# Optimization experiments

Measured on AMD Instinct MI355X. Metric: run time of the kernel, lower is better.

## Reference

```python
import jax, jax.numpy as jnp
import numpy as np

# Model dims: H features, N half-state-size, R low-rank, CH output channels, KL kernel length
H, N, R, CH, KL = 512, 64, 1, 1, 4096


def setup_inputs() -> dict:
    key = jax.random.key(0)
    ks = jax.random.split(key, 8)
    log_dt = jax.random.uniform(ks[0], (H,), minval=float(np.log(1e-3)), maxval=float(np.log(1e-1)), dtype=jnp.float32)
    # Hurwitz-like poles: negative real part, HiPPO-like imaginary ladder
    w_re = -0.5 - jax.random.uniform(ks[1], (H, N), dtype=jnp.float32)
    w_im = jnp.broadcast_to(np.float32(np.pi) * jnp.arange(N, dtype=jnp.float32), (H, N))
    B_re = jax.random.normal(ks[2], (1, H, N), dtype=jnp.float32)
    B_im = jax.random.normal(ks[3], (1, H, N), dtype=jnp.float32)
    # small low-rank correction keeps the Woodbury denominator away from zero
    P_re = 0.1 * jax.random.normal(ks[4], (R, H, N), dtype=jnp.float32)
    P_im = 0.1 * jax.random.normal(ks[5], (R, H, N), dtype=jnp.float32)
    C_re = jax.random.normal(ks[6], (CH, H, N), dtype=jnp.float32)
    C_im = jax.random.normal(ks[7], (CH, H, N), dtype=jnp.float32)
    return dict(log_dt=log_dt, w_re=w_re, w_im=w_im, B_re=B_re, B_im=B_im,
                P_re=P_re, P_im=P_im, C_re=C_re, C_im=C_im, L=KL)


def _kernel(log_dt, w_re, w_im, B_re, B_im, P_re, P_im, C_re, C_im, L):
    dt = jnp.exp(log_dt)                                   # (H,)
    w = (w_re + 1j * w_im) * dt[:, None]                   # (H,N) discretized poles w*dt
    B = B_re + 1j * B_im                                   # (1,H,N)
    P = P_re + 1j * P_im                                   # (R,H,N)
    Q = jnp.conj(P)                                        # hurwitz=False path: Q = conj(P)
    C = C_re + 1j * C_im                                   # (CH,H,N)

    Lf = L // 2 + 1
    kk = jnp.arange(Lf)
    omega = jnp.exp((-2j * np.pi) * kk / L)                # FFT roots of unity (complex64)
    den = 1.0 + omega
    # Nyquist node (omega = -1) handled analytically below; guard the division
    safe_den = jnp.where(jnp.abs(den) < 1e-6, jnp.ones_like(den), den)
    z = 2.0 * (1.0 - omega) / safe_den                     # bilinear-transform nodes

    Bc = jnp.concatenate([B, P], axis=0)                   # (1+R,H,N)
    Cc = jnp.concatenate([C, Q], axis=0)                   # (CH+R,H,N)
    v = Bc[:, None] * Cc[None]                             # (1+R,CH+R,H,N)

    # Cauchy kernel: r[a,b,h,l] = sum_n v[a,b,h,n] / (z[l] - w[h,n])
    recip = 1.0 / (z[None, None, :] - w[:, :, None])       # (H,N,Lf)
    r = jnp.einsum('abhn,hnl->abhl', v, recip)             # (1+R,CH+R,H,Lf)
    r = r * dt[None, None, :, None]

    # rank-1 Woodbury correction
    k_f = r[:-1, :-1] - r[:-1, -1:] * r[-1:, :-1] / (1.0 + r[-1:, -1:])
    k_f = k_f * 2.0 / safe_den

    if L % 2 == 0:
        # analytic z -> inf limit at the Nyquist node: dt/2 * sum_n v00
        nyq = 0.5 * dt[None, None, :] * jnp.sum(v[:-1, :-1], axis=-1)  # (1,CH,H)
        k_f = k_f.at[..., -1].set(nyq)

    k = jnp.fft.irfft(k_f, n=L, axis=-1)[..., :L]          # (1,CH,H,L) real
    return k[-1]                                           # (CH,H,L)


def reference(log_dt, w_re, w_im, B_re, B_im, P_re, P_im, C_re, C_im, L):
    return _kernel(log_dt, w_re, w_im, B_re, B_im, P_re, P_im, C_re, C_im, L)
```

## Files before the change

### kernel.cpp

```cpp
#include <hip/hip_runtime.h>
#include <hip/hip_bf16.h>
#include <math.h>


#define HH   512
#define NN   64
#define LLEN 4096
#define MM   2048
#define NTHREADS 1024
#define ZPAD(i) ((i) + ((i) >> 4))

typedef float v2f __attribute__((ext_vector_type(2)));

__global__ __launch_bounds__(NTHREADS, 8) void ssknplr_kernel(
    const float* __restrict__ log_dt,
    const float* __restrict__ w_re, const float* __restrict__ w_im,
    const float* __restrict__ B_re, const float* __restrict__ B_im,
    const float* __restrict__ P_re, const float* __restrict__ P_im,
    const float* __restrict__ C_re, const float* __restrict__ C_im,
    float* __restrict__ out)
{
    __shared__ v2f    s_pp[NN][10];
    __shared__ float2 s_Z[ZPAD(MM) + 1];

    const int h   = blockIdx.x;
    const int tid = threadIdx.x;

    if (tid < NN) {
        const int n   = tid;
        const int idx = h * NN + n;
        const float dt = expf(log_dt[h]);
        const float wr = w_re[idx] * dt;
        const float wi = w_im[idx] * dt;
        const float Br = B_re[idx], Bi = B_im[idx];
        const float Pr = P_re[idx], Pi = P_im[idx];
        const float Cr = C_re[idx], Ci = C_im[idx];
        const float vals[10] = {
            -wi, -wr, wr * wr,
            dt * (Br * Cr - Bi * Ci),
            dt * (Br * Ci + Bi * Cr),
            dt * (Br * Pr + Bi * Pi),
            dt * (Bi * Pr - Br * Pi),
            dt * (Pr * Cr - Pi * Ci),
            dt * (Pr * Ci + Pi * Cr),
            dt * (Pr * Pr + Pi * Pi)
        };
        #pragma unroll
        for (int j = 0; j < 10; ++j) s_pp[n][j] = (v2f){vals[j], vals[j]};
    }
    __syncthreads();

    v2f tv;
    {
        const float rx = (float)tid * (1.0f / 8192.0f);
        const float ry = (float)(tid + 1024) * (1.0f / 8192.0f);
        tv.x = __builtin_amdgcn_sinf(rx) * __builtin_amdgcn_rcpf(__builtin_amdgcn_cosf(rx));
        tv.y = __builtin_amdgcn_sinf(ry) * __builtin_amdgcn_rcpf(__builtin_amdgcn_cosf(ry));
    }
    const v2f t2v = tv + tv;

    v2f a00r = 0.f, a00i = 0.f, a01r = 0.f, a01i = 0.f;
    v2f a10r = 0.f, a10i = 0.f, a11r = 0.f, a11i = 0.f;

    for (int n = 0; n < NN; ++n) {
        const v2f mwi  = s_pp[n][0];
        const v2f nr   = s_pp[n][1];
        const v2f wr2  = s_pp[n][2];
        const v2f dim = t2v + mwi;
        const v2f den = __builtin_elementwise_fma(dim, dim, wr2);
        const float ip = __builtin_amdgcn_rcpf(den.x * den.y);
        const v2f dsw = __builtin_shufflevector(den, den, 1, 0);
        const v2f inv = dsw * (v2f){ip, ip};
        const v2f ur = nr * inv;
        const v2f ui = -(dim * inv);
        const v2f v00r = s_pp[n][3], v00i = s_pp[n][4];
        const v2f v01r = s_pp[n][5], v01i = s_pp[n][6];
        const v2f v10r = s_pp[n][7], v10i = s_pp[n][8];
        const v2f v11  = s_pp[n][9];
        a00r = __builtin_elementwise_fma( v00r, ur, a00r);
        a00r = __builtin_elementwise_fma(-v00i, ui, a00r);
        a00i = __builtin_elementwise_fma( v00r, ui, a00i);
        a00i = __builtin_elementwise_fma( v00i, ur, a00i);
        a01r = __builtin_elementwise_fma( v01r, ur, a01r);
        a01r = __builtin_elementwise_fma(-v01i, ui, a01r);
        a01i = __builtin_elementwise_fma( v01r, ui, a01i);
        a01i = __builtin_elementwise_fma( v01i, ur, a01i);
        a10r = __builtin_elementwise_fma( v10r, ur, a10r);
        a10r = __builtin_elementwise_fma(-v10i, ui, a10r);
        a10i = __builtin_elementwise_fma( v10r, ui, a10i);
        a10i = __builtin_elementwise_fma( v10i, ur, a10i);
        a11r = __builtin_elementwise_fma( v11,  ur, a11r);
        a11i = __builtin_elementwise_fma( v11,  ui, a11i);
    }

    {
        const v2f dr = a11r + 1.0f;
        const v2f di = a11i;
        const v2f dd = __builtin_elementwise_fma(dr, dr, di * di);
        v2f dinv;
        dinv.x = __builtin_amdgcn_rcpf(dd.x);
        dinv.y = __builtin_amdgcn_rcpf(dd.y);
        const v2f numr = a01r * a10r - a01i * a10i;
        const v2f numi = a01r * a10i + a01i * a10r;
        const v2f cr = (numr * dr + numi * di) * dinv;
        const v2f ci = (numi * dr - numr * di) * dinv;
        const v2f Wr = a00r - cr;
        const v2f Wi = a00i - ci;
        const v2f Kr = __builtin_elementwise_fma(-tv, Wi, Wr);
        const v2f Ki = __builtin_elementwise_fma( tv, Wr, Wi);
        s_Z[ZPAD(tid)] = make_float2(Kr.x, (tid == 0) ? 0.0f : Ki.x);
        s_Z[ZPAD(tid + 1024)] = make_float2(Kr.y, Ki.y);
    }
    if (tid == 0) {
        float sr = 0.f;
        for (int n = 0; n < NN; ++n) sr += s_pp[n][3].x;
        s_Z[ZPAD(MM)] = make_float2(0.5f * sr, 0.0f);
    }
    __syncthreads();

    {
        const int k = tid;
        if (k == 0) {
            const float a = s_Z[ZPAD(0)].x;
            const float b = s_Z[ZPAD(MM)].x;
            s_Z[ZPAD(0)] = make_float2(0.5f * (a + b), 0.5f * (a - b));
            const float2 km = s_Z[ZPAD(MM / 2)];
            s_Z[ZPAD(MM / 2)] = make_float2(km.x, -km.y);
        } else {
            const float2 Ka = s_Z[ZPAD(k)];
            const float2 Kb = s_Z[ZPAD(MM - k)];
            const float rk = (float)k * (1.0f / 4096.0f);
            const float sk = __builtin_amdgcn_sinf(rk);
            const float ck = __builtin_amdgcn_cosf(rk);
            const float Pr = 0.5f * (Ka.x + Kb.x), Pi = 0.5f * (Ka.y - Kb.y);
            const float Dr = 0.5f * (Ka.x - Kb.x), Di = 0.5f * (Ka.y + Kb.y);
            const float al = sk * Dr + ck * Di;
            const float be = ck * Dr - sk * Di;
            s_Z[ZPAD(k)]      = make_float2(Pr - al, Pi + be);
            s_Z[ZPAD(MM - k)] = make_float2(Pr + al, be - Pi);
        }
    }
    __syncthreads();

    for (int s = 10; s >= 1; s -= 2) {
        const int H = 1 << s;
        const int Q = H >> 1;
        const float scale = __builtin_amdgcn_rcpf((float)(2 * H));
        if (tid < 512) {
            const int b    = tid;
            const int j    = b & (Q - 1);
            const int base = ((b >> (s - 1)) << (s + 1)) + j;
            const int i0 = base, i1 = base + Q, i2 = base + H, i3 = base + H + Q;
            const float rev = (float)j * scale;
            const float c  = __builtin_amdgcn_cosf(rev);
            const float sn = __builtin_amdgcn_sinf(rev);
            const float wbr = c * c - sn * sn;
            const float wbi = 2.0f * c * sn;
            const float2 u0 = s_Z[ZPAD(i0)];
            const float2 u1 = s_Z[ZPAD(i1)];
            const float2 u2 = s_Z[ZPAD(i2)];
            const float2 u3 = s_Z[ZPAD(i3)];
            const float a0r = u0.x + u2.x, a0i = u0.y + u2.y;
            const float d0r = u0.x - u2.x, d0i = u0.y - u2.y;
            const float a1r = u1.x + u3.x, a1i = u1.y + u3.y;
            const float d1r = u1.x - u3.x, d1i = u1.y - u3.y;
            const float e0r = d0r * c  - d0i * sn, e0i = d0r * sn + d0i * c;
            const float e1r = -(d1r * sn) - d1i * c, e1i = d1r * c - d1i * sn;
            s_Z[ZPAD(i0)] = make_float2(a0r + a1r, a0i + a1i);
            const float t0r = a0r - a1r, t0i = a0i - a1i;
            s_Z[ZPAD(i1)] = make_float2(t0r * wbr - t0i * wbi, t0r * wbi + t0i * wbr);
            s_Z[ZPAD(i2)] = make_float2(e0r + e1r, e0i + e1i);
            const float t1r = e0r - e1r, t1i = e0i - e1i;
            s_Z[ZPAD(i3)] = make_float2(t1r * wbr - t1i * wbi, t1r * wbi + t1i * wbr);
        }
        __syncthreads();
    }
    {
        const int i0 = tid << 1, i1 = i0 | 1;
        const float2 u = s_Z[ZPAD(i0)];
        const float2 v = s_Z[ZPAD(i1)];
        s_Z[ZPAD(i0)] = make_float2(u.x + v.x, u.y + v.y);
        s_Z[ZPAD(i1)] = make_float2(u.x - v.x, u.y - v.y);
    }
    __syncthreads();

    const float scale = 1.0f / (float)MM;
    float2* o2 = (float2*)out + (size_t)h * MM;
    #pragma unroll
    for (int q = 0; q < 2; ++q) {
        const int m = tid + q * NTHREADS;
        const int r = (int)(__brev((unsigned)m) >> 21);
        const float2 z = s_Z[ZPAD(r)];
        o2[m] = make_float2(z.x * scale, z.y * scale);
    }
}

extern "C" void kernel_launch(void* const* d_in, const int* in_sizes, int n_in,
                              void* d_out, int out_size, void* d_ws, size_t ws_size,
                              hipStream_t stream) {
    const float* log_dt = (const float*)d_in[0];
    const float* w_re   = (const float*)d_in[1];
    const float* w_im   = (const float*)d_in[2];
    const float* B_re   = (const float*)d_in[3];
    const float* B_im   = (const float*)d_in[4];
    const float* P_re   = (const float*)d_in[5];
    const float* P_im   = (const float*)d_in[6];
    const float* C_re   = (const float*)d_in[7];
    const float* C_im   = (const float*)d_in[8];
    float* out = (float*)d_out;

    ssknplr_kernel<<<dim3(HH), dim3(NTHREADS), 0, stream>>>(
        log_dt, w_re, w_im, B_re, B_im, P_re, P_im, C_re, C_im, out);
}
```

Measured before the change: 38.09 us.

## Split into Cauchy kernel and radix-8 register iFFT kernel via workspace

Splits the fused per-head kernel into two launches. A Cauchy kernel uses 1024 blocks of 256 threads, each thread computing four frequency nodes with two independent accumulator sets for more ILP, and writes the spectrum to workspace. A separate inverse-FFT kernel runs radix-8 stages in registers with fewer barriers. This adds a global round trip and a second launch in exchange for smaller blocks and better occupancy, and keeps the fused kernel as a fallback when the workspace is too small.

Result: slower. 42.01 us (+10.3%).

```diff
diff --git a/kernel.cpp b/kernel.cpp
--- a/kernel.cpp
+++ b/kernel.cpp
@@ -7,12 +7,308 @@
 #define NN   64
 #define LLEN 4096
 #define MM   2048
-#define NTHREADS 1024
+#define WS_STRIDE 2056
+#define ZP(i) ((i) + ((i) >> 4) + ((i) >> 8))
 #define ZPAD(i) ((i) + ((i) >> 4))
 
 typedef float v2f __attribute__((ext_vector_type(2)));
 
-__global__ __launch_bounds__(NTHREADS, 8) void ssknplr_kernel(
+__device__ __forceinline__ float sinr(float r) { return __builtin_amdgcn_sinf(r); }
+__device__ __forceinline__ float cosr(float r) { return __builtin_amdgcn_cosf(r); }
+__device__ __forceinline__ float rcpf(float x) { return __builtin_amdgcn_rcpf(x); }
+
+
+__device__ __forceinline__ void cauchy_step(
+    const v2f tv, const v2f mwi, const v2f nr, const v2f wr2,
+    const v2f v00r, const v2f v00i, const v2f v01r, const v2f v01i,
+    const v2f v10r, const v2f v10i, const v2f v11,
+    v2f& a00r, v2f& a00i, v2f& a01r, v2f& a01i,
+    v2f& a10r, v2f& a10i, v2f& a11r, v2f& a11i)
+{
+    const v2f dim = __builtin_elementwise_fma(tv, (v2f){2.0f, 2.0f}, mwi);
+    const v2f den = __builtin_elementwise_fma(dim, dim, wr2);
+    const float ip = rcpf(den.x * den.y);
+    v2f inv; inv.x = den.y * ip; inv.y = den.x * ip;
+    const v2f ur = nr * inv;
+    const v2f ui = -(dim * inv);
+    a00r = __builtin_elementwise_fma( v00r, ur, a00r);
+    a00r = __builtin_elementwise_fma(-v00i, ui, a00r);
+    a00i = __builtin_elementwise_fma( v00r, ui, a00i);
+    a00i = __builtin_elementwise_fma( v00i, ur, a00i);
+    a01r = __builtin_elementwise_fma( v01r, ur, a01r);
+    a01r = __builtin_elementwise_fma(-v01i, ui, a01r);
+    a01i = __builtin_elementwise_fma( v01r, ui, a01i);
+    a01i = __builtin_elementwise_fma( v01i, ur, a01i);
+    a10r = __builtin_elementwise_fma( v10r, ur, a10r);
+    a10r = __builtin_elementwise_fma(-v10i, ui, a10r);
+    a10i = __builtin_elementwise_fma( v10r, ui, a10i);
+    a10i = __builtin_elementwise_fma( v10i, ur, a10i);
+    a11r = __builtin_elementwise_fma( v11,  ur, a11r);
+    a11i = __builtin_elementwise_fma( v11,  ui, a11i);
+}
+
+__device__ __forceinline__ void woodbury_K(
+    const v2f tv,
+    const v2f a00r, const v2f a00i, const v2f a01r, const v2f a01i,
+    const v2f a10r, const v2f a10i, const v2f a11r, const v2f a11i,
+    v2f& Kr, v2f& Ki)
+{
+    const v2f dr = a11r + 1.0f;
+    const v2f di = a11i;
+    const v2f dd = __builtin_elementwise_fma(dr, dr, di * di);
+    v2f dinv; dinv.x = rcpf(dd.x); dinv.y = rcpf(dd.y);
+    const v2f numr = a01r * a10r - a01i * a10i;
+    const v2f numi = a01r * a10i + a01i * a10r;
+    const v2f cr = (numr * dr + numi * di) * dinv;
+    const v2f ci = (numi * dr - numr * di) * dinv;
+    const v2f Wr = a00r - cr;
+    const v2f Wi = a00i - ci;
+    Kr = __builtin_elementwise_fma(-tv, Wi, Wr);
+    Ki = __builtin_elementwise_fma( tv, Wr, Wi);
+}
+
+__global__ __launch_bounds__(256, 6) void cauchy_kernel(
+    const float* __restrict__ log_dt,
+    const float* __restrict__ w_re, const float* __restrict__ w_im,
+    const float* __restrict__ B_re, const float* __restrict__ B_im,
+    const float* __restrict__ P_re, const float* __restrict__ P_im,
+    const float* __restrict__ C_re, const float* __restrict__ C_im,
+    float2* __restrict__ Kout)
+{
+    __shared__ float4 s_p4[NN][5];
+
+    const int blk   = blockIdx.x;
+    const int h     = blk >> 1;
+    const int chunk = blk & 1;
+    const int tid   = threadIdx.x;
+
+    if (tid < NN) {
+        const int n   = tid;
+        const int idx = h * NN + n;
+        const float dt = expf(log_dt[h]);
+        const float wr = w_re[idx] * dt;
+        const float wi = w_im[idx] * dt;
+        const float Br = B_re[idx], Bi = B_im[idx];
+        const float Pr = P_re[idx], Pi = P_im[idx];
+        const float Cr = C_re[idx], Ci = C_im[idx];
+        const float v00r = dt * (Br * Cr - Bi * Ci);
+        const float v00i = dt * (Br * Ci + Bi * Cr);
+        const float v01r = dt * (Br * Pr + Bi * Pi);
+        const float v01i = dt * (Bi * Pr - Br * Pi);
+        const float v10r = dt * (Pr * Cr - Pi * Ci);
+        const float v10i = dt * (Pr * Ci + Pi * Cr);
+        const float v11  = dt * (Pr * Pr + Pi * Pi);
+        s_p4[n][0] = make_float4(-wi, -wi, -wr, -wr);
+        s_p4[n][1] = make_float4(wr * wr, wr * wr, v00r, v00r);
+        s_p4[n][2] = make_float4(v00i, v00i, v01r, v01r);
+        s_p4[n][3] = make_float4(v01i, v01i, v10r, v10r);
+        s_p4[n][4] = make_float4(v10i, v10i, v11, v11);
+    }
+    __syncthreads();
+
+    const int l0 = chunk * 256 + tid;
+    v2f tvA, tvB;
+    {
+        const float rA0 = (float)l0            * (1.0f / 8192.0f);
+        const float rA1 = (float)(l0 + 1024)   * (1.0f / 8192.0f);
+        const float rB0 = (float)(l0 + 512)    * (1.0f / 8192.0f);
+        const float rB1 = (float)(l0 + 1536)   * (1.0f / 8192.0f);
+        tvA.x = sinr(rA0) * rcpf(cosr(rA0));
+        tvA.y = sinr(rA1) * rcpf(cosr(rA1));
+        tvB.x = sinr(rB0) * rcpf(cosr(rB0));
+        tvB.y = sinr(rB1) * rcpf(cosr(rB1));
+    }
+
+    v2f A00r = 0.f, A00i = 0.f, A01r = 0.f, A01i = 0.f;
+    v2f A10r = 0.f, A10i = 0.f, A11r = 0.f, A11i = 0.f;
+    v2f B00r = 0.f, B00i = 0.f, B01r = 0.f, B01i = 0.f;
+    v2f B10r = 0.f, B10i = 0.f, B11r = 0.f, B11i = 0.f;
+
+    for (int n = 0; n < NN; ++n) {
+        const float4 f0 = s_p4[n][0];
+        const float4 f1 = s_p4[n][1];
+        const float4 f2 = s_p4[n][2];
+        const float4 f3 = s_p4[n][3];
+        const float4 f4 = s_p4[n][4];
+        const v2f mwi  = {f0.x, f0.y}, nr   = {f0.z, f0.w};
+        const v2f wr2  = {f1.x, f1.y}, v00r = {f1.z, f1.w};
+        const v2f v00i = {f2.x, f2.y}, v01r = {f2.z, f2.w};
+        const v2f v01i = {f3.x, f3.y}, v10r = {f3.z, f3.w};
+        const v2f v10i = {f4.x, f4.y}, v11  = {f4.z, f4.w};
+        cauchy_step(tvA, mwi, nr, wr2, v00r, v00i, v01r, v01i, v10r, v10i, v11,
+                    A00r, A00i, A01r, A01i, A10r, A10i, A11r, A11i);
+        cauchy_step(tvB, mwi, nr, wr2, v00r, v00i, v01r, v01i, v10r, v10i, v11,
+                    B00r, B00i, B01r, B01i, B10r, B10i, B11r, B11i);
+    }
+
+    float2* __restrict__ Kh = Kout + (size_t)h * WS_STRIDE;
+    {
+        v2f Kr, Ki;
+        woodbury_K(tvA, A00r, A00i, A01r, A01i, A10r, A10i, A11r, A11i, Kr, Ki);
+        Kh[l0]        = make_float2(Kr.x, (l0 == 0) ? 0.0f : Ki.x);
+        Kh[l0 + 1024] = make_float2(Kr.y, Ki.y);
+    }
+    {
+        v2f Kr, Ki;
+        woodbury_K(tvB, B00r, B00i, B01r, B01i, B10r, B10i, B11r, B11i, Kr, Ki);
+        Kh[l0 + 512]  = make_float2(Kr.x, Ki.x);
+        Kh[l0 + 1536] = make_float2(Kr.y, Ki.y);
+    }
+    if (chunk == 0 && tid == 0) {
+        float sr = 0.f;
+        for (int n = 0; n < NN; ++n) sr += s_p4[n][1].z;
+        Kh[MM] = make_float2(0.5f * sr, 0.0f);
+    }
+}
+
+
+__device__ __forceinline__ void radix8(float xr[8], float xi[8], const float rev)
+{
+    const float c   = cosr(rev), s = sinr(rev);
+    const float w2r = c * c - s * s, w2i = 2.0f * c * s;
+    const float w4r = w2r * w2r - w2i * w2i;
+    const float w4i = 2.0f * w2r * w2i;
+    const float RH  = 0.70710678118654752440f;
+    const float cms = RH * (c - s), cps = RH * (c + s);
+
+    const float Ar0 = xr[0] + xr[4], Ai0 = xi[0] + xi[4];
+    const float Ar1 = xr[1] + xr[5], Ai1 = xi[1] + xi[5];
+    const float Ar2 = xr[2] + xr[6], Ai2 = xi[2] + xi[6];
+    const float Ar3 = xr[3] + xr[7], Ai3 = xi[3] + xi[7];
+    float dr, di;
+    dr = xr[0] - xr[4]; di = xi[0] - xi[4];
+    const float Br0 = dr * c - di * s,      Bi0 = dr * s + di * c;
+    dr = xr[1] - xr[5]; di = xi[1] - xi[5];
+    const float Br1 = dr * cms - di * cps,  Bi1 = dr * cps + di * cms;
+    dr = xr[2] - xr[6]; di = xi[2] - xi[6];
+    const float Br2 = -dr * s - di * c,     Bi2 = dr * c - di * s;
+    dr = xr[3] - xr[7]; di = xi[3] - xi[7];
+    const float Br3 = -dr * cps - di * cms, Bi3 = dr * cms - di * cps;
+
+    const float Cr0 = Ar0 + Ar2, Ci0 = Ai0 + Ai2;
+    const float Cr1 = Ar1 + Ar3, Ci1 = Ai1 + Ai3;
+    dr = Ar0 - Ar2; di = Ai0 - Ai2;
+    const float Dr0 = dr * w2r - di * w2i,  Di0 = dr * w2i + di * w2r;
+    dr = Ar1 - Ar3; di = Ai1 - Ai3;
+    const float Dr1 = -dr * w2i - di * w2r, Di1 = dr * w2r - di * w2i;
+    const float Er0 = Br0 + Br2, Ei0 = Bi0 + Bi2;
+    const float Er1 = Br1 + Br3, Ei1 = Bi1 + Bi3;
+    dr = Br0 - Br2; di = Bi0 - Bi2;
+    const float Fr0 = dr * w2r - di * w2i,  Fi0 = dr * w2i + di * w2r;
+    dr = Br1 - Br3; di = Bi1 - Bi3;
+    const float Fr1 = -dr * w2i - di * w2r, Fi1 = dr * w2r - di * w2i;
+
+    xr[0] = Cr0 + Cr1; xi[0] = Ci0 + Ci1;
+    dr = Cr0 - Cr1; di = Ci0 - Ci1;
+    xr[1] = dr * w4r - di * w4i; xi[1] = dr * w4i + di * w4r;
+    xr[2] = Dr0 + Dr1; xi[2] = Di0 + Di1;
+    dr = Dr0 - Dr1; di = Di0 - Di1;
+    xr[3] = dr * w4r - di * w4i; xi[3] = dr * w4i + di * w4r;
+    xr[4] = Er0 + Er1; xi[4] = Ei0 + Ei1;
+    dr = Er0 - Er1; di = Ei0 - Ei1;
+    xr[5] = dr * w4r - di * w4i; xi[5] = dr * w4i + di * w4r;
+    xr[6] = Fr0 + Fr1; xi[6] = Fi0 + Fi1;
+    dr = Fr0 - Fr1; di = Fi0 - Fi1;
+    xr[7] = dr * w4r - di * w4i; xi[7] = dr * w4i + di * w4r;
+}
+
+__global__ __launch_bounds__(256, 2) void ifft_kernel(
+    const float2* __restrict__ Kg, float* __restrict__ out)
+{
+    __shared__ float2 s_Z[ZP(MM - 1) + 1];
+
+    const int h = blockIdx.x;
+    const int t = threadIdx.x;
+    const float2* __restrict__ Kh = Kg + (size_t)h * WS_STRIDE;
+
+    float xr[8], xi[8];
+
+    #pragma unroll
+    for (int q = 0; q < 8; ++q) {
+        const int m = t + (q << 8);
+        const float2 Ka = Kh[m];
+        const float2 Kb = Kh[MM - m];
+        const float rev = (float)m * (1.0f / 4096.0f);
+        const float sk = sinr(rev), ck = cosr(rev);
+        const float Pr = 0.5f * (Ka.x + Kb.x), Pi = 0.5f * (Ka.y - Kb.y);
+        const float Dr = 0.5f * (Ka.x - Kb.x), Di = 0.5f * (Ka.y + Kb.y);
+        xr[q] = Pr - (sk * Dr + ck * Di);
+        xi[q] = Pi + (ck * Dr - sk * Di);
+    }
+    radix8(xr, xi, (float)t * (1.0f / 2048.0f));
+    #pragma unroll
+    for (int q = 0; q < 8; ++q) {
+        const int i = t + (q << 8);
+        s_Z[ZP(i)] = make_float2(xr[q], xi[q]);
+    }
+    __syncthreads();
+
+    {
+        const int base = ((t >> 5) << 8) + (t & 31);
+        #pragma unroll
+        for (int q = 0; q < 8; ++q) {
+            const float2 z = s_Z[ZP(base + (q << 5))];
+            xr[q] = z.x; xi[q] = z.y;
+        }
+        radix8(xr, xi, (float)(t & 31) * (1.0f / 256.0f));
+        #pragma unroll
+        for (int q = 0; q < 8; ++q)
+            s_Z[ZP(base + (q << 5))] = make_float2(xr[q], xi[q]);
+    }
+    __syncthreads();
+
+    {
+        const int base = ((t >> 2) << 5) + (t & 3);
+        #pragma unroll
+        for (int q = 0; q < 8; ++q) {
+            const float2 z = s_Z[ZP(base + (q << 2))];
+            xr[q] = z.x; xi[q] = z.y;
+        }
+        radix8(xr, xi, (float)(t & 3) * (1.0f / 32.0f));
+        #pragma unroll
+        for (int q = 0; q < 8; ++q)
+            s_Z[ZP(base + (q << 2))] = make_float2(xr[q], xi[q]);
+    }
+    __syncthreads();
+
+    {
+        const int i0 = t << 3;
+        #pragma unroll
+        for (int q = 0; q < 8; ++q) {
+            const float2 z = s_Z[ZP(i0 + q)];
+            xr[q] = z.x; xi[q] = z.y;
+        }
+        #pragma unroll
+        for (int g = 0; g < 2; ++g) {
+            const int o = g * 4;
+            const float A0r = xr[o] + xr[o+2], A0i = xi[o] + xi[o+2];
+            const float A1r = xr[o+1] + xr[o+3], A1i = xi[o+1] + xi[o+3];
+            const float B0r = xr[o] - xr[o+2], B0i = xi[o] - xi[o+2];
+            const float B1r = -(xi[o+1] - xi[o+3]);
+            const float B1i =  (xr[o+1] - xr[o+3]);
+            xr[o]   = A0r + A1r; xi[o]   = A0i + A1i;
+            xr[o+1] = A0r - A1r; xi[o+1] = A0i - A1i;
+            xr[o+2] = B0r + B1r; xi[o+2] = B0i + B1i;
+            xr[o+3] = B0r - B1r; xi[o+3] = B0i - B1i;
+        }
+        #pragma unroll
+        for (int q = 0; q < 8; ++q)
+            s_Z[ZP(i0 + q)] = make_float2(xr[q], xi[q]);
+    }
+    __syncthreads();
+
+    const float scale = 1.0f / (float)MM;
+    float2* o2 = (float2*)out + (size_t)h * MM;
+    #pragma unroll
+    for (int q = 0; q < 8; ++q) {
+        const int m = t + (q << 8);
+        const int r = (int)(__brev((unsigned)m) >> 21);
+        const float2 z = s_Z[ZP(r)];
+        o2[m] = make_float2(z.x * scale, z.y * scale);
+    }
+}
+
+__global__ __launch_bounds__(1024, 8) void ssknplr_fused(
     const float* __restrict__ log_dt,
     const float* __restrict__ w_re, const float* __restrict__ w_im,
     const float* __restrict__ B_re, const float* __restrict__ B_im,
@@ -37,12 +333,9 @@
         const float Cr = C_re[idx], Ci = C_im[idx];
         const float vals[10] = {
             -wi, -wr, wr * wr,
-            dt * (Br * Cr - Bi * Ci),
-            dt * (Br * Ci + Bi * Cr),
-            dt * (Br * Pr + Bi * Pi),
-            dt * (Bi * Pr - Br * Pi),
-            dt * (Pr * Cr - Pi * Ci),
-            dt * (Pr * Ci + Pi * Cr),
+            dt * (Br * Cr - Bi * Ci), dt * (Br * Ci + Bi * Cr),
+            dt * (Br * Pr + Bi * Pi), dt * (Bi * Pr - Br * Pi),
+            dt * (Pr * Cr - Pi * Ci), dt * (Pr * Ci + Pi * Cr),
             dt * (Pr * Pr + Pi * Pi)
         };
         #pragma unroll
@@ -54,60 +347,19 @@
     {
         const float rx = (float)tid * (1.0f / 8192.0f);
         const float ry = (float)(tid + 1024) * (1.0f / 8192.0f);
-        tv.x = __builtin_amdgcn_sinf(rx) * __builtin_amdgcn_rcpf(__builtin_amdgcn_cosf(rx));
-        tv.y = __builtin_amdgcn_sinf(ry) * __builtin_amdgcn_rcpf(__builtin_amdgcn_cosf(ry));
-    }
-    const v2f t2v = tv + tv;
-
+        tv.x = sinr(rx) * rcpf(cosr(rx));
+        tv.y = sinr(ry) * rcpf(cosr(ry));
+    }
     v2f a00r = 0.f, a00i = 0.f, a01r = 0.f, a01i = 0.f;
     v2f a10r = 0.f, a10i = 0.f, a11r = 0.f, a11i = 0.f;
-
     for (int n = 0; n < NN; ++n) {
-        const v2f mwi  = s_pp[n][0];
-        const v2f nr   = s_pp[n][1];
-        const v2f wr2  = s_pp[n][2];
-        const v2f dim = t2v + mwi;
-        const v2f den = __builtin_elementwise_fma(dim, dim, wr2);
-        const float ip = __builtin_amdgcn_rcpf(den.x * den.y);
-        const v2f dsw = __builtin_shufflevector(den, den, 1, 0);
-        const v2f inv = dsw * (v2f){ip, ip};
-        const v2f ur = nr * inv;
-        const v2f ui = -(dim * inv);
-        const v2f v00r = s_pp[n][3], v00i = s_pp[n][4];
-        const v2f v01r = s_pp[n][5], v01i = s_pp[n][6];
-        const v2f v10r = s_pp[n][7], v10i = s_pp[n][8];
-        const v2f v11  = s_pp[n][9];
-        a00r = __builtin_elementwise_fma( v00r, ur, a00r);
-        a00r = __builtin_elementwise_fma(-v00i, ui, a00r);
-        a00i = __builtin_elementwise_fma( v00r, ui, a00i);
-        a00i = __builtin_elementwise_fma( v00i, ur, a00i);
-        a01r = __builtin_elementwise_fma( v01r, ur, a01r);
-        a01r = __builtin_elementwise_fma(-v01i, ui, a01r);
-        a01i = __builtin_elementwise_fma( v01r, ui, a01i);
-        a01i = __builtin_elementwise_fma( v01i, ur, a01i);
-        a10r = __builtin_elementwise_fma( v10r, ur, a10r);
-        a10r = __builtin_elementwise_fma(-v10i, ui, a10r);
-        a10i = __builtin_elementwise_fma( v10r, ui, a10i);
-        a10i = __builtin_elementwise_fma( v10i, ur, a10i);
-        a11r = __builtin_elementwise_fma( v11,  ur, a11r);
-        a11i = __builtin_elementwise_fma( v11,  ui, a11i);
-    }
-
-    {
-        const v2f dr = a11r + 1.0f;
-        const v2f di = a11i;
-        const v2f dd = __builtin_elementwise_fma(dr, dr, di * di);
-        v2f dinv;
-        dinv.x = __builtin_amdgcn_rcpf(dd.x);
-        dinv.y = __builtin_amdgcn_rcpf(dd.y);
-        const v2f numr = a01r * a10r - a01i * a10i;
-        const v2f numi = a01r * a10i + a01i * a10r;
-        const v2f cr = (numr * dr + numi * di) * dinv;
-        const v2f ci = (numi * dr - numr * di) * dinv;
-        const v2f Wr = a00r - cr;
-        const v2f Wi = a00i - ci;
-        const v2f Kr = __builtin_elementwise_fma(-tv, Wi, Wr);
-        const v2f Ki = __builtin_elementwise_fma( tv, Wr, Wi);
+        cauchy_step(tv, s_pp[n][0], s_pp[n][1], s_pp[n][2], s_pp[n][3], s_pp[n][4],
+                    s_pp[n][5], s_pp[n][6], s_pp[n][7], s_pp[n][8], s_pp[n][9],
+                    a00r, a00i, a01r, a01i, a10r, a10i, a11r, a11i);
+    }
+    {
+        v2f Kr, Ki;
+        woodbury_K(tv, a00r, a00i, a01r, a01i, a10r, a10i, a11r, a11i, Kr, Ki);
         s_Z[ZPAD(tid)] = make_float2(Kr.x, (tid == 0) ? 0.0f : Ki.x);
         s_Z[ZPAD(tid + 1024)] = make_float2(Kr.y, Ki.y);
     }
@@ -130,8 +382,7 @@
             const float2 Ka = s_Z[ZPAD(k)];
             const float2 Kb = s_Z[ZPAD(MM - k)];
             const float rk = (float)k * (1.0f / 4096.0f);
-            const float sk = __builtin_amdgcn_sinf(rk);
-            const float ck = __builtin_amdgcn_cosf(rk);
+            const float sk = sinr(rk), ck = cosr(rk);
             const float Pr = 0.5f * (Ka.x + Kb.x), Pi = 0.5f * (Ka.y - Kb.y);
             const float Dr = 0.5f * (Ka.x - Kb.x), Di = 0.5f * (Ka.y + Kb.y);
             const float al = sk * Dr + ck * Di;
@@ -143,17 +394,17 @@
     __syncthreads();
 
     for (int s = 10; s >= 1; s -= 2) {
-        const int H = 1 << s;
-        const int Q = H >> 1;
-        const float scale = __builtin_amdgcn_rcpf((float)(2 * H));
+        const int Hh = 1 << s;
+        const int Q = Hh >> 1;
+        const float sc = rcpf((float)(2 * Hh));
         if (tid < 512) {
             const int b    = tid;
             const int j    = b & (Q - 1);
             const int base = ((b >> (s - 1)) << (s + 1)) + j;
-            const int i0 = base, i1 = base + Q, i2 = base + H, i3 = base + H + Q;
-            const float rev = (float)j * scale;
-            const float c  = __builtin_amdgcn_cosf(rev);
-            const float sn = __builtin_amdgcn_sinf(rev);
+            const int i0 = base, i1 = base + Q, i2 = base + Hh, i3 = base + Hh + Q;
+            const float rev = (float)j * sc;
+            const float c  = cosr(rev);
+            const float sn = sinr(rev);
             const float wbr = c * c - sn * sn;
             const float wbi = 2.0f * c * sn;
             const float2 u0 = s_Z[ZPAD(i0)];
@@ -164,7 +415,7 @@
             const float d0r = u0.x - u2.x, d0i = u0.y - u2.y;
             const float a1r = u1.x + u3.x, a1i = u1.y + u3.y;
             const float d1r = u1.x - u3.x, d1i = u1.y - u3.y;
-            const float e0r = d0r * c  - d0i * sn, e0i = d0r * sn + d0i * c;
+            const float e0r = d0r * c - d0i * sn, e0i = d0r * sn + d0i * c;
             const float e1r = -(d1r * sn) - d1i * c, e1i = d1r * c - d1i * sn;
             s_Z[ZPAD(i0)] = make_float2(a0r + a1r, a0i + a1i);
             const float t0r = a0r - a1r, t0i = a0i - a1i;
@@ -188,7 +439,7 @@
     float2* o2 = (float2*)out + (size_t)h * MM;
     #pragma unroll
     for (int q = 0; q < 2; ++q) {
-        const int m = tid + q * NTHREADS;
+        const int m = tid + q * 1024;
         const int r = (int)(__brev((unsigned)m) >> 21);
         const float2 z = s_Z[ZPAD(r)];
         o2[m] = make_float2(z.x * scale, z.y * scale);
@@ -209,6 +460,14 @@
     const float* C_im   = (const float*)d_in[8];
     float* out = (float*)d_out;
 
-    ssknplr_kernel<<<dim3(HH), dim3(NTHREADS), 0, stream>>>(
-        log_dt, w_re, w_im, B_re, B_im, P_re, P_im, C_re, C_im, out);
-}
+    const size_t need = (size_t)HH * WS_STRIDE * sizeof(float2);
+    if (ws_size >= need) {
+        float2* Kws = (float2*)d_ws;
+        cauchy_kernel<<<dim3(HH * 2), dim3(256), 0, stream>>>(
+            log_dt, w_re, w_im, B_re, B_im, P_re, P_im, C_re, C_im, Kws);
+        ifft_kernel<<<dim3(HH), dim3(256), 0, stream>>>(Kws, out);
+    } else {
+        ssknplr_fused<<<dim3(HH), dim3(1024), 0, stream>>>(
+            log_dt, w_re, w_im, B_re, B_im, P_re, P_im, C_re, C_im, out);
+    }
+}
```
